# Performance work log

Measured on AMD Instinct MI355X. Metric: run time of the kernel, lower is better.

The kernel has to match this reference:

```python
import jax, jax.numpy as jnp
import numpy as np

V = 50000
D = 128
EF = 16
E = 800000
LN_EPS = 1e-5


def setup_inputs() -> dict:
    key = jax.random.key(0)
    ks = jax.random.split(key, 9)
    h = jax.random.normal(ks[0], (V, D), dtype=jnp.float32)
    edge_index = jax.random.randint(ks[1], (2, E), 0, V, dtype=jnp.int64)
    edge_attr = jax.random.normal(ks[2], (E, EF), dtype=jnp.float32)
    # msg_mlp = Linear(D+EF, D) -> ReLU -> Dropout(0) -> Linear(D, D)
    s1 = 1.0 / np.sqrt(D + EF)
    s2 = 1.0 / np.sqrt(D)
    W1 = jax.random.uniform(ks[3], (D + EF, D), minval=-s1, maxval=s1, dtype=jnp.float32)
    b1 = jax.random.uniform(ks[4], (D,), minval=-s1, maxval=s1, dtype=jnp.float32)
    W2 = jax.random.uniform(ks[5], (D, D), minval=-s2, maxval=s2, dtype=jnp.float32)
    b2 = jax.random.uniform(ks[6], (D,), minval=-s2, maxval=s2, dtype=jnp.float32)
    gamma = jnp.ones((D,), dtype=jnp.float32)
    beta = jnp.zeros((D,), dtype=jnp.float32)
    return {"h": h, "edge_index": edge_index, "edge_attr": edge_attr,
            "W1": W1, "b1": b1, "W2": W2, "b2": b2,
            "gamma": gamma, "beta": beta}


def _layer_norm(x, gamma, beta):
    mu = jnp.mean(x, axis=-1, keepdims=True)
    var = jnp.mean(jnp.square(x - mu), axis=-1, keepdims=True)
    return (x - mu) * jax.lax.rsqrt(var + LN_EPS) * gamma + beta


def reference(h, edge_index, edge_attr, W1, b1, W2, b2, gamma, beta):
    src, dst = edge_index[0], edge_index[1]
    # gather source node features, concat edge features: [E, D+EF]
    x = jnp.concatenate([h[src], edge_attr], axis=-1)
    # per-edge message MLP (dropout p=0 -> identity)
    msg = jax.nn.relu(x @ W1 + b1) @ W2 + b2  # [E, D]
    # scatter-add messages to destinations
    agg = jax.ops.segment_sum(msg, dst, num_segments=V)  # [V, D]
    # count initialized to ones BEFORE scatter_add -> denominator = 1 + in_degree
    deg = jax.ops.segment_sum(jnp.ones((E,), dtype=h.dtype), dst, num_segments=V)
    count = (1.0 + deg)[:, None]  # [V, 1]
    return _layer_norm(h + agg / count, gamma, beta)
```

## Files before the change

### kernel.cpp

```cpp
#include <hip/hip_runtime.h>
#include <hip/hip_bf16.h>

#define V 50000
#define D 128
#define EF 16
#define E_EDGES 800000
#define NT 12500
#define USTR 136
#define XESTR 40
#define CSTR 136
#define NSCAN 196
#define EGRID 1024
#define UGRID 782

typedef __attribute__((ext_vector_type(8))) __bf16 bf16x8;
typedef __attribute__((ext_vector_type(4))) float f32x4;
typedef __attribute__((ext_vector_type(2))) __fp16 fp16x2;

__device__ inline unsigned short f2bf(float f) {
    unsigned u = __float_as_uint(f);
    u += 0x7FFF + ((u >> 16) & 1);
    return (unsigned short)(u >> 16);
}
__device__ inline unsigned pack2(float a, float b) {
    return (unsigned)f2bf(a) | ((unsigned)f2bf(b) << 16);
}
__device__ inline float bf2f(unsigned short u) {
    return __uint_as_float((unsigned)u << 16);
}
__device__ inline unsigned pkbf(float a, float b) {
    union { __hip_bfloat162 h; unsigned u; } v;
    v.h = __float22bfloat162_rn(make_float2(a, b));
    return v.u;
}
__device__ inline unsigned pkf16(float a, float b) {
    union { fp16x2 h; unsigned u; } v;
    v.h = __builtin_amdgcn_cvt_pkrtz(a, b);
    return v.u;
}

__global__ __launch_bounds__(256)
void setup_kernel(const int* __restrict__ ei, int* __restrict__ cnt,
                  float* __restrict__ agg,
                  const float* __restrict__ W1, const float* __restrict__ W2,
                  unsigned short* __restrict__ W1p, unsigned short* __restrict__ W2p) {
    int idx = blockIdx.x * 256 + threadIdx.x;
    *(float4*)(agg + ((size_t)idx << 2)) = (float4){0.f, 0.f, 0.f, 0.f};
    if (idx < E_EDGES) atomicAdd(&cnt[ei[E_EDGES + idx]], 1);
    if (idx < 5 * 128 * 32) {
        int kb = idx >> 12, rem = idx & 4095;
        int n = rem >> 5, kk = rem & 31;
        int k = kb * 32 + kk;
        W1p[idx] = f2bf((k < D + EF) ? W1[k * D + n] : 0.0f);
    }
    if (idx < 4 * 128 * 32) {
        int kb = idx >> 12, rem = idx & 4095;
        int n = rem >> 5, kk = rem & 31;
        W2p[idx] = f2bf(W2[(kb * 32 + kk) * D + n]);
    }
}

__global__ __launch_bounds__(256)
void u_gemm_kernel(const float* __restrict__ h,
                   const unsigned short* __restrict__ W1p,
                   unsigned short* __restrict__ U) {
    __shared__ __align__(16) unsigned short Hs[64 * USTR];
    const int tid  = threadIdx.x;
    const int lane = tid & 63;
    const int wave = tid >> 6;
    const int nlo  = lane & 15;
    const int kq   = lane >> 4;
    const int er   = tid >> 4;
    const int ec   = tid & 15;
    const int gbase = blockIdx.x << 6;

    bf16x8 B1[4][2];
    #pragma unroll
    for (int t = 0; t < 2; ++t) {
        int n = wave * 32 + t * 16 + nlo;
        #pragma unroll
        for (int kb = 0; kb < 4; ++kb)
            B1[kb][t] = *(const bf16x8*)(W1p + ((kb << 7) + n) * 32 + (kq << 3));
    }

    #pragma unroll
    for (int m = 0; m < 4; ++m) {
        int row = er + m * 16;
        int grow = gbase + row;
        unsigned* o = (unsigned*)(Hs + row * USTR + (ec << 3));
        if (grow < V) {
            const float4* p = (const float4*)(h + (size_t)grow * D + (ec << 3));
            float4 v0 = p[0], v1 = p[1];
            o[0] = pack2(v0.x, v0.y); o[1] = pack2(v0.z, v0.w);
            o[2] = pack2(v1.x, v1.y); o[3] = pack2(v1.z, v1.w);
        } else {
            o[0] = 0u; o[1] = 0u; o[2] = 0u; o[3] = 0u;
        }
    }
    __syncthreads();

    f32x4 acc[4][2];
    #pragma unroll
    for (int mt = 0; mt < 4; ++mt)
        #pragma unroll
        for (int t = 0; t < 2; ++t)
            acc[mt][t] = (f32x4){0.f, 0.f, 0.f, 0.f};

    #pragma unroll
    for (int kb = 0; kb < 4; ++kb) {
        bf16x8 A[4];
        int ko = kb * 32 + (kq << 3);
        #pragma unroll
        for (int mt = 0; mt < 4; ++mt)
            A[mt] = *(const bf16x8*)(Hs + (mt * 16 + nlo) * USTR + ko);
        #pragma unroll
        for (int mt = 0; mt < 4; ++mt)
            #pragma unroll
            for (int t = 0; t < 2; ++t)
                acc[mt][t] = __builtin_amdgcn_mfma_f32_16x16x32_bf16(A[mt], B1[kb][t], acc[mt][t], 0, 0, 0);
    }

    #pragma unroll
    for (int mt = 0; mt < 4; ++mt)
        #pragma unroll
        for (int t = 0; t < 2; ++t)
            #pragma unroll
            for (int r = 0; r < 4; ++r) {
                int row = mt * 16 + (kq << 2) + r;
                int grow = gbase + row;
                int col = wave * 32 + t * 16 + nlo;
                if (grow < V)
                    U[(size_t)grow * D + col] = f2bf(acc[mt][t][r]);
            }
}

__device__ inline int block_excl_scan(int x, int t, int* ws) {
    int lane = t & 63, w = t >> 6;
    int inc = x;
    #pragma unroll
    for (int off = 1; off < 64; off <<= 1) {
        int y = __shfl_up(inc, off);
        if (lane >= off) inc += y;
    }
    if (lane == 63) ws[w] = inc;
    __syncthreads();
    if (t == 0) {
        int r = 0;
        #pragma unroll
        for (int i = 0; i < 4; ++i) { int c = ws[i]; ws[i] = r; r += c; }
    }
    __syncthreads();
    return inc - x + ws[w];
}

__global__ __launch_bounds__(256)
void scan1_kernel(const int* __restrict__ cnt, int* __restrict__ cursor,
                  int* __restrict__ bsum) {
    __shared__ int ws[4];
    __shared__ int tot;
    int t = threadIdx.x;
    int i = blockIdx.x * 256 + t;
    int x = (i < V) ? cnt[i] : 0;
    int ex = block_excl_scan(x, t, ws);
    if (i < V) cursor[i] = ex;
    if (t == 255) tot = ex + x;
    __syncthreads();
    if (t == 0) bsum[blockIdx.x] = tot;
}

__global__ __launch_bounds__(256)
void scatter_kernel(const int* __restrict__ ei, int* __restrict__ cursor,
                    const int* __restrict__ bsum,
                    int* __restrict__ srcs, int* __restrict__ dsts,
                    int* __restrict__ eidx) {
    __shared__ int ws[4];
    __shared__ int sboff[NSCAN];
    int t = threadIdx.x;
    int x = (t < NSCAN) ? bsum[t] : 0;
    int ex = block_excl_scan(x, t, ws);
    if (t < NSCAN) sboff[t] = ex;
    __syncthreads();
    int e = blockIdx.x * 256 + t;
    int d = ei[E_EDGES + e];
    int pos = atomicAdd(&cursor[d], 1) + sboff[d >> 8];
    srcs[pos] = ei[e];
    dsts[pos] = d;
    eidx[pos] = e;
}

__global__ __launch_bounds__(256, 4)
void edge_kernel(const unsigned short* __restrict__ U,
                 const float* __restrict__ ea,
                 const int* __restrict__ srcs, const int* __restrict__ dsts,
                 const int* __restrict__ eidx,
                 const unsigned short* __restrict__ W1p, const unsigned short* __restrict__ W2p,
                 const float* __restrict__ b1, const float* __restrict__ b2,
                 float* __restrict__ agg) {
    __shared__ __align__(16) unsigned short Us[64 * USTR];
    __shared__ __align__(16) _Float16 Cs[64 * CSTR];
    __shared__ __align__(16) unsigned short Xe[64 * XESTR];
    __shared__ int sDst[2][64];

    const int tid  = threadIdx.x;
    const int lane = tid & 63;
    const int wave = tid >> 6;
    const int nlo  = lane & 15;
    const int kq   = lane >> 4;
    const int er   = tid >> 4;
    const int ec   = tid & 15;
    const int ee   = tid >> 2;
    const int eq   = tid & 3;

    bf16x8 B1e[2], B2[4][2];
    float4 b1n[2], b2n[2];
    #pragma unroll
    for (int t = 0; t < 2; ++t) {
        int n = wave * 32 + t * 16 + nlo;
        b1n[t] = *(const float4*)(b1 + wave * 32 + t * 16 + (kq << 2));
        b2n[t] = *(const float4*)(b2 + wave * 32 + t * 16 + (kq << 2));
        B1e[t] = *(const bf16x8*)(W1p + ((4 << 7) + n) * 32 + (kq << 3));
        #pragma unroll
        for (int kb = 0; kb < 4; ++kb)
            B2[kb][t] = *(const bf16x8*)(W2p + ((kb << 7) + n) * 32 + (kq << 3));
    }

    {
        unsigned* xz = (unsigned*)Xe;
        int i0 = tid, i1 = tid + 256;
        xz[(i0 >> 3) * (XESTR / 2) + 8 + (i0 & 7)] = 0u;
        xz[(i1 >> 3) * (XESTR / 2) + 8 + (i1 & 7)] = 0u;
    }

    const int base0 = blockIdx.x << 6;
    int a0 = srcs[base0 + er];
    int a1 = srcs[base0 + er + 16];
    int a2 = srcs[base0 + er + 32];
    int a3 = srcs[base0 + er + 48];
    int aev = eidx[base0 + ee];
    int ddcur = dsts[base0 + lane];
    bf16x8 pf0 = *(const bf16x8*)(U + (size_t)a0 * D + (ec << 3));
    bf16x8 pf1 = *(const bf16x8*)(U + (size_t)a1 * D + (ec << 3));
    bf16x8 pf2 = *(const bf16x8*)(U + (size_t)a2 * D + (ec << 3));
    bf16x8 pf3 = *(const bf16x8*)(U + (size_t)a3 * D + (ec << 3));
    float4 pfe = *(const float4*)(ea + (size_t)aev * EF + (eq << 2));

    int n1 = blockIdx.x + EGRID;
    int nb1 = (n1 < NT ? n1 : blockIdx.x) << 6;
    int i1s0 = srcs[nb1 + er];
    int i1s1 = srcs[nb1 + er + 16];
    int i1s2 = srcs[nb1 + er + 32];
    int i1s3 = srcs[nb1 + er + 48];
    int i1e  = eidx[nb1 + ee];
    int i1d  = dsts[nb1 + lane];

    int buf = 0;
    for (int tile = blockIdx.x; tile < NT; tile += EGRID) {
        if (tid < 64) sDst[buf][tid] = ddcur;
        *(bf16x8*)(Us + er * USTR + (ec << 3))        = pf0;
        *(bf16x8*)(Us + (er + 16) * USTR + (ec << 3)) = pf1;
        *(bf16x8*)(Us + (er + 32) * USTR + (ec << 3)) = pf2;
        *(bf16x8*)(Us + (er + 48) * USTR + (ec << 3)) = pf3;
        {
            unsigned* xp = (unsigned*)Xe + ee * (XESTR / 2) + (eq << 1);
            xp[0] = pkbf(pfe.x, pfe.y);
            xp[1] = pkbf(pfe.z, pfe.w);
        }
        __syncthreads();

        f32x4 accE[4][2];
        #pragma unroll
        for (int mt = 0; mt < 4; ++mt)
            #pragma unroll
            for (int t = 0; t < 2; ++t) {
                uint2 uu = *(const uint2*)(Us + (mt * 16 + nlo) * USTR + wave * 32 + t * 16 + (kq << 2));
                accE[mt][t][0] = bf2f((unsigned short)uu.x);
                accE[mt][t][1] = bf2f((unsigned short)(uu.x >> 16));
                accE[mt][t][2] = bf2f((unsigned short)uu.y);
                accE[mt][t][3] = bf2f((unsigned short)(uu.y >> 16));
            }
        {
            bf16x8 Xf[4];
            #pragma unroll
            for (int mt = 0; mt < 4; ++mt)
                Xf[mt] = *(const bf16x8*)(Xe + (mt * 16 + nlo) * XESTR + (kq << 3));
            #pragma unroll
            for (int mt = 0; mt < 4; ++mt)
                #pragma unroll
                for (int t = 0; t < 2; ++t)
                    accE[mt][t] = __builtin_amdgcn_mfma_f32_16x16x32_bf16(B1e[t], Xf[mt], accE[mt][t], 0, 0, 0);
        }

        #pragma unroll
        for (int mt = 0; mt < 4; ++mt)
            #pragma unroll
            for (int t = 0; t < 2; ++t) {
                uint2 yw;
                yw.x = pkbf(fmaxf(accE[mt][t][0] + b1n[t].x, 0.0f),
                            fmaxf(accE[mt][t][1] + b1n[t].y, 0.0f));
                yw.y = pkbf(fmaxf(accE[mt][t][2] + b1n[t].z, 0.0f),
                            fmaxf(accE[mt][t][3] + b1n[t].w, 0.0f));
                *(uint2*)(Us + (mt * 16 + nlo) * USTR + wave * 32 + t * 16 + (kq << 2)) = yw;
            }
        __syncthreads();

        f32x4 acc2[4][2];
        #pragma unroll
        for (int mt = 0; mt < 4; ++mt)
            #pragma unroll
            for (int t = 0; t < 2; ++t)
                acc2[mt][t] = (f32x4){0.f, 0.f, 0.f, 0.f};

        #pragma unroll
        for (int kb = 0; kb < 4; ++kb) {
            bf16x8 Yf[4];
            int ko = kb * 32 + (kq << 3);
            #pragma unroll
            for (int mt = 0; mt < 4; ++mt)
                Yf[mt] = *(const bf16x8*)(Us + (mt * 16 + nlo) * USTR + ko);
            #pragma unroll
            for (int mt = 0; mt < 4; ++mt)
                #pragma unroll
                for (int t = 0; t < 2; ++t)
                    acc2[mt][t] = __builtin_amdgcn_mfma_f32_16x16x32_bf16(B2[kb][t], Yf[mt], acc2[mt][t], 0, 0, 0);
        }

        #pragma unroll
        for (int mt = 0; mt < 4; ++mt)
            #pragma unroll
            for (int t = 0; t < 2; ++t) {
                uint2 cw;
                cw.x = pkf16(acc2[mt][t][0] + b2n[t].x, acc2[mt][t][1] + b2n[t].y);
                cw.y = pkf16(acc2[mt][t][2] + b2n[t].z, acc2[mt][t][3] + b2n[t].w);
                *(uint2*)((unsigned short*)Cs + (size_t)(mt * 16 + nlo) * CSTR + wave * 32 + t * 16 + (kq << 2)) = cw;
            }
        __syncthreads();

        int n2 = tile + 2 * EGRID;
        int nb2 = (n2 < NT ? n2 : tile) << 6;
        int i2s0 = srcs[nb2 + er];
        int i2s1 = srcs[nb2 + er + 16];
        int i2s2 = srcs[nb2 + er + 32];
        int i2s3 = srcs[nb2 + er + 48];
        int i2e  = eidx[nb2 + ee];
        int i2d  = dsts[nb2 + lane];

        bf16x8 q0 = *(const bf16x8*)(U + (size_t)i1s0 * D + (ec << 3));
        bf16x8 q1 = *(const bf16x8*)(U + (size_t)i1s1 * D + (ec << 3));
        bf16x8 q2 = *(const bf16x8*)(U + (size_t)i1s2 * D + (ec << 3));
        bf16x8 q3 = *(const bf16x8*)(U + (size_t)i1s3 * D + (ec << 3));
        float4 qe = *(const float4*)(ea + (size_t)i1e * EF + (eq << 2));
        int nextdd = i1d;

        {
            int col = tid & 127;
            int rbase = (tid >> 7) << 5;
            float sum = 0.f;
            int cur = sDst[buf][rbase];
            for (int i = 0; i < 32; ++i) {
                int d = sDst[buf][rbase + i];
                if (d != cur) {
                    atomicAdd(&agg[(size_t)cur * D + col], sum);
                    sum = 0.f;
                    cur = d;
                }
                sum += (float)Cs[(rbase + i) * CSTR + col];
            }
            atomicAdd(&agg[(size_t)cur * D + col], sum);
        }

        pf0 = q0; pf1 = q1; pf2 = q2; pf3 = q3; pfe = qe; ddcur = nextdd;
        i1s0 = i2s0; i1s1 = i2s1; i1s2 = i2s2; i1s3 = i2s3; i1e = i2e; i1d = i2d;
        buf ^= 1;
    }
}

__global__ __launch_bounds__(256)
void finalize_kernel(const float* __restrict__ h, const float* __restrict__ agg,
                     const int* __restrict__ cnt,
                     const float* __restrict__ gamma, const float* __restrict__ beta,
                     float* __restrict__ out) {
    int wave = threadIdx.x >> 6, lane = threadIdx.x & 63;
    int v = blockIdx.x * 4 + wave;
    if (v >= V) return;
    float inv = 1.0f / (1.0f + (float)cnt[v]);
    const float* hr = h + (size_t)v * D;
    const float* ar = agg + (size_t)v * D;
    float x0 = hr[lane]      + ar[lane]      * inv;
    float x1 = hr[lane + 64] + ar[lane + 64] * inv;
    float s = x0 + x1;
    #pragma unroll
    for (int m = 32; m; m >>= 1) s += __shfl_xor(s, m);
    float mu = s * (1.0f / 128.0f);
    float d0 = x0 - mu, d1 = x1 - mu;
    float vs = d0 * d0 + d1 * d1;
    #pragma unroll
    for (int m = 32; m; m >>= 1) vs += __shfl_xor(vs, m);
    float rs = rsqrtf(vs * (1.0f / 128.0f) + 1e-5f);
    out[(size_t)v * D + lane]      = d0 * rs * gamma[lane]      + beta[lane];
    out[(size_t)v * D + 64 + lane] = d1 * rs * gamma[lane + 64] + beta[lane + 64];
}

extern "C" void kernel_launch(void* const* d_in, const int* in_sizes, int n_in,
                              void* d_out, int out_size, void* d_ws, size_t ws_size,
                              hipStream_t stream) {
    const float* h     = (const float*)d_in[0];
    const int*   ei    = (const int*)d_in[1];
    const float* ea    = (const float*)d_in[2];
    const float* W1    = (const float*)d_in[3];
    const float* b1    = (const float*)d_in[4];
    const float* W2    = (const float*)d_in[5];
    const float* b2    = (const float*)d_in[6];
    const float* gamma = (const float*)d_in[7];
    const float* beta  = (const float*)d_in[8];
    float* out = (float*)d_out;

    char* ws = (char*)d_ws;
    float*          agg    = (float*)ws;
    int*            cnt    = (int*)(ws + 25600000);
    int*            cursor = (int*)(ws + 25800000);
    int*            bsum   = (int*)(ws + 26000000);
    int*            srcs   = (int*)(ws + 26000800);
    int*            dsts   = (int*)(ws + 29200800);
    int*            eidx   = (int*)(ws + 32400800);
    unsigned short* W1p    = (unsigned short*)(ws + 35600800);
    unsigned short* W2p    = (unsigned short*)(ws + 35641760);
    unsigned short* U      = (unsigned short*)(ws + 35674528);

    (void)hipMemsetAsync(cnt, 0, 200000, stream);
    setup_kernel<<<6250, 256, 0, stream>>>(ei, cnt, agg, W1, W2, W1p, W2p);
    u_gemm_kernel<<<UGRID, 256, 0, stream>>>(h, W1p, U);
    scan1_kernel<<<NSCAN, 256, 0, stream>>>(cnt, cursor, bsum);
    scatter_kernel<<<3125, 256, 0, stream>>>(ei, cursor, bsum, srcs, dsts, eidx);
    edge_kernel<<<EGRID, 256, 0, stream>>>(U, ea, srcs, dsts, eidx, W1p, W2p, b1, b2, agg);
    finalize_kernel<<<12500, 256, 0, stream>>>(h, agg, cnt, gamma, beta, out);
}
```

Before: 311.3 us.

## Fuse U-GEMM into setup kernel and drop sorted src/dst arrays

Merges the node-projection GEMM into the setup kernel. The first blocks build their W1 bf16 fragments straight from fp32 W1 instead of reading the packed copy, which saves one launch and the dependency on W1p. The scatter kernel now writes only the sorted edge-index permutation, and the edge kernel gathers src and dst through ei[eidx]. The edge kernel also issues the next tile's index loads earlier in the loop to hide the extra level of indirection. This removes two 3.2 MB writes and their reads, at the cost of an extra dependent random gather per edge and a heavier setup kernel.

```diff
diff --git a/kernel.cpp b/kernel.cpp
--- a/kernel.cpp
+++ b/kernel.cpp
@@ -40,11 +40,14 @@
 }
 
 __global__ __launch_bounds__(256)
-void setup_kernel(const int* __restrict__ ei, int* __restrict__ cnt,
-                  float* __restrict__ agg,
+void setup_kernel(const float* __restrict__ h, const int* __restrict__ ei,
+                  int* __restrict__ cnt, float* __restrict__ agg,
                   const float* __restrict__ W1, const float* __restrict__ W2,
-                  unsigned short* __restrict__ W1p, unsigned short* __restrict__ W2p) {
-    int idx = blockIdx.x * 256 + threadIdx.x;
+                  unsigned short* __restrict__ W1p, unsigned short* __restrict__ W2p,
+                  unsigned short* __restrict__ U) {
+    __shared__ __align__(16) unsigned short Hs[64 * USTR];
+    const int tid = threadIdx.x;
+    int idx = blockIdx.x * 256 + tid;
     *(float4*)(agg + ((size_t)idx << 2)) = (float4){0.f, 0.f, 0.f, 0.f};
     if (idx < E_EDGES) atomicAdd(&cnt[ei[E_EDGES + idx]], 1);
     if (idx < 5 * 128 * 32) {
@@ -58,14 +61,8 @@
         int n = rem >> 5, kk = rem & 31;
         W2p[idx] = f2bf(W2[(kb * 32 + kk) * D + n]);
     }
-}
-
-__global__ __launch_bounds__(256)
-void u_gemm_kernel(const float* __restrict__ h,
-                   const unsigned short* __restrict__ W1p,
-                   unsigned short* __restrict__ U) {
-    __shared__ __align__(16) unsigned short Hs[64 * USTR];
-    const int tid  = threadIdx.x;
+    if (blockIdx.x >= UGRID) return;
+
     const int lane = tid & 63;
     const int wave = tid >> 6;
     const int nlo  = lane & 15;
@@ -79,8 +76,13 @@
     for (int t = 0; t < 2; ++t) {
         int n = wave * 32 + t * 16 + nlo;
         #pragma unroll
-        for (int kb = 0; kb < 4; ++kb)
-            B1[kb][t] = *(const bf16x8*)(W1p + ((kb << 7) + n) * 32 + (kq << 3));
+        for (int kb = 0; kb < 4; ++kb) {
+            union { bf16x8 v; unsigned short s[8]; } f;
+            #pragma unroll
+            for (int j = 0; j < 8; ++j)
+                f.s[j] = f2bf(W1[(kb * 32 + (kq << 3) + j) * D + n]);
+            B1[kb][t] = f.v;
+        }
     }
 
     #pragma unroll
@@ -170,9 +172,7 @@
 
 __global__ __launch_bounds__(256)
 void scatter_kernel(const int* __restrict__ ei, int* __restrict__ cursor,
-                    const int* __restrict__ bsum,
-                    int* __restrict__ srcs, int* __restrict__ dsts,
-                    int* __restrict__ eidx) {
+                    const int* __restrict__ bsum, int* __restrict__ eidx) {
     __shared__ int ws[4];
     __shared__ int sboff[NSCAN];
     int t = threadIdx.x;
@@ -183,16 +183,13 @@
     int e = blockIdx.x * 256 + t;
     int d = ei[E_EDGES + e];
     int pos = atomicAdd(&cursor[d], 1) + sboff[d >> 8];
-    srcs[pos] = ei[e];
-    dsts[pos] = d;
     eidx[pos] = e;
 }
 
 __global__ __launch_bounds__(256, 4)
 void edge_kernel(const unsigned short* __restrict__ U,
                  const float* __restrict__ ea,
-                 const int* __restrict__ srcs, const int* __restrict__ dsts,
-                 const int* __restrict__ eidx,
+                 const int* __restrict__ ei, const int* __restrict__ eidx,
                  const unsigned short* __restrict__ W1p, const unsigned short* __restrict__ W2p,
                  const float* __restrict__ b1, const float* __restrict__ b2,
                  float* __restrict__ agg) {
@@ -232,26 +229,28 @@
     }
 
     const int base0 = blockIdx.x << 6;
-    int a0 = srcs[base0 + er];
-    int a1 = srcs[base0 + er + 16];
-    int a2 = srcs[base0 + er + 32];
-    int a3 = srcs[base0 + er + 48];
-    int aev = eidx[base0 + ee];
-    int ddcur = dsts[base0 + lane];
+    int e0a = eidx[base0 + er];
+    int e0b = eidx[base0 + er + 16];
+    int e0c = eidx[base0 + er + 32];
+    int e0d = eidx[base0 + er + 48];
+    int e0e = eidx[base0 + ee];
+    int e0l = eidx[base0 + lane];
+    int a0 = ei[e0a], a1 = ei[e0b], a2 = ei[e0c], a3 = ei[e0d];
+    int ddcur = ei[E_EDGES + e0l];
     bf16x8 pf0 = *(const bf16x8*)(U + (size_t)a0 * D + (ec << 3));
     bf16x8 pf1 = *(const bf16x8*)(U + (size_t)a1 * D + (ec << 3));
     bf16x8 pf2 = *(const bf16x8*)(U + (size_t)a2 * D + (ec << 3));
     bf16x8 pf3 = *(const bf16x8*)(U + (size_t)a3 * D + (ec << 3));
-    float4 pfe = *(const float4*)(ea + (size_t)aev * EF + (eq << 2));
+    float4 pfe = *(const float4*)(ea + (size_t)e0e * EF + (eq << 2));
 
     int n1 = blockIdx.x + EGRID;
     int nb1 = (n1 < NT ? n1 : blockIdx.x) << 6;
-    int i1s0 = srcs[nb1 + er];
-    int i1s1 = srcs[nb1 + er + 16];
-    int i1s2 = srcs[nb1 + er + 32];
-    int i1s3 = srcs[nb1 + er + 48];
-    int i1e  = eidx[nb1 + ee];
-    int i1d  = dsts[nb1 + lane];
+    int e1a = eidx[nb1 + er];
+    int e1b = eidx[nb1 + er + 16];
+    int e1c = eidx[nb1 + er + 32];
+    int e1d = eidx[nb1 + er + 48];
+    int e1e = eidx[nb1 + ee];
+    int e1l = eidx[nb1 + lane];
 
     int buf = 0;
     for (int tile = blockIdx.x; tile < NT; tile += EGRID) {
@@ -303,6 +302,17 @@
             }
         __syncthreads();
 
+        int n2 = tile + 2 * EGRID;
+        int nb2 = (n2 < NT ? n2 : tile) << 6;
+        int e2a = eidx[nb2 + er];
+        int e2b = eidx[nb2 + er + 16];
+        int e2c = eidx[nb2 + er + 32];
+        int e2d = eidx[nb2 + er + 48];
+        int e2e = eidx[nb2 + ee];
+        int e2l = eidx[nb2 + lane];
+        int s1a = ei[e1a], s1b = ei[e1b], s1c = ei[e1c], s1d = ei[e1d];
+        int d1  = ei[E_EDGES + e1l];
+
         f32x4 acc2[4][2];
         #pragma unroll
         for (int mt = 0; mt < 4; ++mt)
@@ -335,21 +345,11 @@
             }
         __syncthreads();
 
-        int n2 = tile + 2 * EGRID;
-        int nb2 = (n2 < NT ? n2 : tile) << 6;
-        int i2s0 = srcs[nb2 + er];
-        int i2s1 = srcs[nb2 + er + 16];
-        int i2s2 = srcs[nb2 + er + 32];
-        int i2s3 = srcs[nb2 + er + 48];
-        int i2e  = eidx[nb2 + ee];
-        int i2d  = dsts[nb2 + lane];
-
-        bf16x8 q0 = *(const bf16x8*)(U + (size_t)i1s0 * D + (ec << 3));
-        bf16x8 q1 = *(const bf16x8*)(U + (size_t)i1s1 * D + (ec << 3));
-        bf16x8 q2 = *(const bf16x8*)(U + (size_t)i1s2 * D + (ec << 3));
-        bf16x8 q3 = *(const bf16x8*)(U + (size_t)i1s3 * D + (ec << 3));
-        float4 qe = *(const float4*)(ea + (size_t)i1e * EF + (eq << 2));
-        int nextdd = i1d;
+        bf16x8 q0 = *(const bf16x8*)(U + (size_t)s1a * D + (ec << 3));
+        bf16x8 q1 = *(const bf16x8*)(U + (size_t)s1b * D + (ec << 3));
+        bf16x8 q2 = *(const bf16x8*)(U + (size_t)s1c * D + (ec << 3));
+        bf16x8 q3 = *(const bf16x8*)(U + (size_t)s1d * D + (ec << 3));
+        float4 qe = *(const float4*)(ea + (size_t)e1e * EF + (eq << 2));
 
         {
             int col = tid & 127;
@@ -368,8 +368,8 @@
             atomicAdd(&agg[(size_t)cur * D + col], sum);
         }
 
-        pf0 = q0; pf1 = q1; pf2 = q2; pf3 = q3; pfe = qe; ddcur = nextdd;
-        i1s0 = i2s0; i1s1 = i2s1; i1s2 = i2s2; i1s3 = i2s3; i1e = i2e; i1d = i2d;
+        pf0 = q0; pf1 = q1; pf2 = q2; pf3 = q3; pfe = qe; ddcur = d1;
+        e1a = e2a; e1b = e2b; e1c = e2c; e1d = e2d; e1e = e2e; e1l = e2l;
         buf ^= 1;
     }
 }
@@ -419,18 +419,15 @@
     int*            cnt    = (int*)(ws + 25600000);
     int*            cursor = (int*)(ws + 25800000);
     int*            bsum   = (int*)(ws + 26000000);
-    int*            srcs   = (int*)(ws + 26000800);
-    int*            dsts   = (int*)(ws + 29200800);
-    int*            eidx   = (int*)(ws + 32400800);
-    unsigned short* W1p    = (unsigned short*)(ws + 35600800);
-    unsigned short* W2p    = (unsigned short*)(ws + 35641760);
-    unsigned short* U      = (unsigned short*)(ws + 35674528);
+    int*            eidx   = (int*)(ws + 26000800);
+    unsigned short* W1p    = (unsigned short*)(ws + 29200800);
+    unsigned short* W2p    = (unsigned short*)(ws + 29241760);
+    unsigned short* U      = (unsigned short*)(ws + 29274528);
 
     (void)hipMemsetAsync(cnt, 0, 200000, stream);
-    setup_kernel<<<6250, 256, 0, stream>>>(ei, cnt, agg, W1, W2, W1p, W2p);
-    u_gemm_kernel<<<UGRID, 256, 0, stream>>>(h, W1p, U);
+    setup_kernel<<<6250, 256, 0, stream>>>(h, ei, cnt, agg, W1, W2, W1p, W2p, U);
     scan1_kernel<<<NSCAN, 256, 0, stream>>>(cnt, cursor, bsum);
-    scatter_kernel<<<3125, 256, 0, stream>>>(ei, cursor, bsum, srcs, dsts, eidx);
-    edge_kernel<<<EGRID, 256, 0, stream>>>(U, ea, srcs, dsts, eidx, W1p, W2p, b1, b2, agg);
+    scatter_kernel<<<3125, 256, 0, stream>>>(ei, cursor, bsum, eidx);
+    edge_kernel<<<EGRID, 256, 0, stream>>>(U, ea, ei, eidx, W1p, W2p, b1, b2, agg);
     finalize_kernel<<<12500, 256, 0, stream>>>(h, agg, cnt, gamma, beta, out);
 }
```

New measurement: 315.9 us. About the same (+1.5%).

## Deepen gather prefetch pipeline to two tiles ahead of compute

Applied to the files above, without the earlier changes.

Extends the software pipeline in the edge MLP kernel so the gathered node rows and edge features are loaded two tiles ahead instead of one, and edge indices three tiles ahead. The index loads for the far tile are issued between the two GEMM stages. The aim is to hide more of the random-gather latency behind MFMA work. In exchange it holds extra bf16x8 vectors in registers, which may lower occupancy or cause spills.

```diff
diff --git a/kernel.cpp b/kernel.cpp
--- a/kernel.cpp
+++ b/kernel.cpp
@@ -232,30 +232,46 @@
     }
 
     const int base0 = blockIdx.x << 6;
-    int a0 = srcs[base0 + er];
-    int a1 = srcs[base0 + er + 16];
-    int a2 = srcs[base0 + er + 32];
-    int a3 = srcs[base0 + er + 48];
-    int aev = eidx[base0 + ee];
-    int ddcur = dsts[base0 + lane];
-    bf16x8 pf0 = *(const bf16x8*)(U + (size_t)a0 * D + (ec << 3));
-    bf16x8 pf1 = *(const bf16x8*)(U + (size_t)a1 * D + (ec << 3));
-    bf16x8 pf2 = *(const bf16x8*)(U + (size_t)a2 * D + (ec << 3));
-    bf16x8 pf3 = *(const bf16x8*)(U + (size_t)a3 * D + (ec << 3));
-    float4 pfe = *(const float4*)(ea + (size_t)aev * EF + (eq << 2));
+    int dd0 = dsts[base0 + lane];
+    {
+    }
+    int t0a = srcs[base0 + er];
+    int t0b = srcs[base0 + er + 16];
+    int t0c = srcs[base0 + er + 32];
+    int t0d = srcs[base0 + er + 48];
+    int t0e = eidx[base0 + ee];
+    bf16x8 pf0 = *(const bf16x8*)(U + (size_t)t0a * D + (ec << 3));
+    bf16x8 pf1 = *(const bf16x8*)(U + (size_t)t0b * D + (ec << 3));
+    bf16x8 pf2 = *(const bf16x8*)(U + (size_t)t0c * D + (ec << 3));
+    bf16x8 pf3 = *(const bf16x8*)(U + (size_t)t0d * D + (ec << 3));
+    float4 pfe = *(const float4*)(ea + (size_t)t0e * EF + (eq << 2));
 
     int n1 = blockIdx.x + EGRID;
     int nb1 = (n1 < NT ? n1 : blockIdx.x) << 6;
-    int i1s0 = srcs[nb1 + er];
-    int i1s1 = srcs[nb1 + er + 16];
-    int i1s2 = srcs[nb1 + er + 32];
-    int i1s3 = srcs[nb1 + er + 48];
-    int i1e  = eidx[nb1 + ee];
-    int i1d  = dsts[nb1 + lane];
+    int dd1 = dsts[nb1 + lane];
+    int t1a = srcs[nb1 + er];
+    int t1b = srcs[nb1 + er + 16];
+    int t1c = srcs[nb1 + er + 32];
+    int t1d = srcs[nb1 + er + 48];
+    int t1e = eidx[nb1 + ee];
+    bf16x8 qf0 = *(const bf16x8*)(U + (size_t)t1a * D + (ec << 3));
+    bf16x8 qf1 = *(const bf16x8*)(U + (size_t)t1b * D + (ec << 3));
+    bf16x8 qf2 = *(const bf16x8*)(U + (size_t)t1c * D + (ec << 3));
+    bf16x8 qf3 = *(const bf16x8*)(U + (size_t)t1d * D + (ec << 3));
+    float4 qfe = *(const float4*)(ea + (size_t)t1e * EF + (eq << 2));
+
+    int n2 = blockIdx.x + 2 * EGRID;
+    int nb2 = (n2 < NT ? n2 : blockIdx.x) << 6;
+    int i2a = srcs[nb2 + er];
+    int i2b = srcs[nb2 + er + 16];
+    int i2c = srcs[nb2 + er + 32];
+    int i2d = srcs[nb2 + er + 48];
+    int i2e = eidx[nb2 + ee];
+    int dd2 = dsts[nb2 + lane];
 
     int buf = 0;
     for (int tile = blockIdx.x; tile < NT; tile += EGRID) {
-        if (tid < 64) sDst[buf][tid] = ddcur;
+        if (tid < 64) sDst[buf][tid] = dd0;
         *(bf16x8*)(Us + er * USTR + (ec << 3))        = pf0;
         *(bf16x8*)(Us + (er + 16) * USTR + (ec << 3)) = pf1;
         *(bf16x8*)(Us + (er + 32) * USTR + (ec << 3)) = pf2;
@@ -303,6 +319,15 @@
             }
         __syncthreads();
 
+        int n3 = tile + 3 * EGRID;
+        int nb3 = (n3 < NT ? n3 : tile) << 6;
+        int i3a = srcs[nb3 + er];
+        int i3b = srcs[nb3 + er + 16];
+        int i3c = srcs[nb3 + er + 32];
+        int i3d = srcs[nb3 + er + 48];
+        int i3e = eidx[nb3 + ee];
+        int dd3 = dsts[nb3 + lane];
+
         f32x4 acc2[4][2];
         #pragma unroll
         for (int mt = 0; mt < 4; ++mt)
@@ -335,21 +360,11 @@
             }
         __syncthreads();
 
-        int n2 = tile + 2 * EGRID;
-        int nb2 = (n2 < NT ? n2 : tile) << 6;
-        int i2s0 = srcs[nb2 + er];
-        int i2s1 = srcs[nb2 + er + 16];
-        int i2s2 = srcs[nb2 + er + 32];
-        int i2s3 = srcs[nb2 + er + 48];
-        int i2e  = eidx[nb2 + ee];
-        int i2d  = dsts[nb2 + lane];
-
-        bf16x8 q0 = *(const bf16x8*)(U + (size_t)i1s0 * D + (ec << 3));
-        bf16x8 q1 = *(const bf16x8*)(U + (size_t)i1s1 * D + (ec << 3));
-        bf16x8 q2 = *(const bf16x8*)(U + (size_t)i1s2 * D + (ec << 3));
-        bf16x8 q3 = *(const bf16x8*)(U + (size_t)i1s3 * D + (ec << 3));
-        float4 qe = *(const float4*)(ea + (size_t)i1e * EF + (eq << 2));
-        int nextdd = i1d;
+        bf16x8 rf0 = *(const bf16x8*)(U + (size_t)i2a * D + (ec << 3));
+        bf16x8 rf1 = *(const bf16x8*)(U + (size_t)i2b * D + (ec << 3));
+        bf16x8 rf2 = *(const bf16x8*)(U + (size_t)i2c * D + (ec << 3));
+        bf16x8 rf3 = *(const bf16x8*)(U + (size_t)i2d * D + (ec << 3));
+        float4 rfe = *(const float4*)(ea + (size_t)i2e * EF + (eq << 2));
 
         {
             int col = tid & 127;
@@ -368,8 +383,10 @@
             atomicAdd(&agg[(size_t)cur * D + col], sum);
         }
 
-        pf0 = q0; pf1 = q1; pf2 = q2; pf3 = q3; pfe = qe; ddcur = nextdd;
-        i1s0 = i2s0; i1s1 = i2s1; i1s2 = i2s2; i1s3 = i2s3; i1e = i2e; i1d = i2d;
+        pf0 = qf0; pf1 = qf1; pf2 = qf2; pf3 = qf3; pfe = qfe;
+        qf0 = rf0; qf1 = rf1; qf2 = rf2; qf3 = rf3; qfe = rfe;
+        dd0 = dd1; dd1 = dd2; dd2 = dd3;
+        i2a = i3a; i2b = i3b; i2c = i3c; i2d = i3d; i2e = i3e;
         buf ^= 1;
     }
 }
```

Result: slower. 376.1 us (+20.8%).
